# Performance work log

Measured on AMD Instinct MI355X. Metric: run time of the kernel, lower is better.

The kernel has to match this reference:

```python
import jax, jax.numpy as jnp
import numpy as np

N = 50000
E = 800000
D = 128
L = 2


def setup_inputs() -> dict:
    key = jax.random.key(0)
    ks = jax.random.split(key, 8)
    x = jax.random.normal(ks[0], (N, D), dtype=jnp.float32)
    edge_index = jax.random.randint(ks[1], (2, E), 0, N, dtype=jnp.int64)
    s = 1.0 / np.sqrt(D)
    Wl = jax.random.uniform(ks[2], (L, D, D), jnp.float32, -s, s)  # neighbor transform (with bias)
    bl = jax.random.uniform(ks[3], (L, D), jnp.float32, -s, s)
    Wr = jax.random.uniform(ks[4], (L, D, D), jnp.float32, -s, s)  # root/self transform (no bias)
    W = jax.random.uniform(ks[5], (D, D), jnp.float32, -s, s)      # final Linear
    b = jax.random.uniform(ks[6], (D,), jnp.float32, -s, s)
    return {"x": x, "edge_index": edge_index, "Wl": Wl, "bl": bl, "Wr": Wr, "W": W, "b": b}


def reference(x, edge_index, Wl, bl, Wr, W, b):
    src, dst = edge_index[0], edge_index[1]
    n = x.shape[0]
    for l in range(Wl.shape[0]):
        # gather neighbor (source) features, scatter-max into destination nodes
        agg = jax.ops.segment_max(x[src], dst, num_segments=n)  # [N, D]
        agg = jnp.where(jnp.isneginf(agg), 0.0, agg)  # PyG: isolated nodes -> 0
        # SAGEConv: lin_l(agg) + lin_r(x)
        x = agg @ Wl[l].T + bl[l] + x @ Wr[l].T
        x = jax.nn.relu(x)
    return x @ W.T + b
```

## Files before the change

### kernel.cpp

```cpp
#include <hip/hip_runtime.h>
#include <math.h>

#define NN 50000
#define NE 800000
#define DD 128
#define NBUCK 196
#define PTILE 4096
#define PBLOCKS 196
#define CONVB 6250
#define LHS 136

typedef unsigned short u16;
typedef short s8v __attribute__((ext_vector_type(8)));
typedef float f16v __attribute__((ext_vector_type(16)));

__device__ __forceinline__ u16 f2bf(float f) {
    unsigned u = __float_as_uint(f);
    return (u16)((u + 0x7FFFu + ((u >> 16) & 1u)) >> 16);
}
__device__ __forceinline__ float bflo(unsigned u) { return __uint_as_float(u << 16); }
__device__ __forceinline__ float bfhi(unsigned u) { return __uint_as_float(u & 0xFFFF0000u); }

__device__ __forceinline__ void pack_one(const float* __restrict__ Wl,
                                         const float* __restrict__ Wr,
                                         bool two, int o, u16* __restrict__ out) {
    int j = o & 7;
    int l = (o >> 3) & 63;
    int cn = o >> 9;
    int n = cn & 3;
    int c = cn >> 2;
    int colj = n * 32 + (l & 31);
    int k = c * 16 + (l >> 5) * 8 + j;
    float v;
    if (two) v = (k < DD) ? Wl[colj * DD + k] : Wr[colj * DD + (k - DD)];
    else     v = Wl[colj * DD + k];
    out[o] = f2bf(v);
}

__global__ __launch_bounds__(256) void prep_kernel(
        const int* __restrict__ ei, int* __restrict__ bcnt,
        const float4* __restrict__ x4, ushort4* __restrict__ hbx,
        const float* __restrict__ Wl, const float* __restrict__ Wr,
        const float* __restrict__ W,
        u16* __restrict__ Bpk0, u16* __restrict__ Bpk1, u16* __restrict__ Bpkf) {
    int bid = blockIdx.x;
    int tid = threadIdx.x;
    if (bid < PBLOCKS) {
        __shared__ int h[NBUCK];
        for (int i = tid; i < NBUCK; i += 256) h[i] = 0;
        __syncthreads();
        int e0 = bid * PTILE;
#pragma unroll
        for (int i = 0; i < 16; i++) {
            int e = e0 + i * 256 + tid;
            if (e < NE) atomicAdd(&h[ei[NE + e] >> 8], 1);
        }
        __syncthreads();
        for (int i = tid; i < NBUCK; i += 256)
            if (h[i]) atomicAdd(&bcnt[i], h[i]);
    } else if (bid < PBLOCKS + CONVB) {
        int i = (bid - PBLOCKS) * 256 + tid;
        float4 v = x4[i];
        ushort4 o;
        o.x = f2bf(v.x); o.y = f2bf(v.y); o.z = f2bf(v.z); o.w = f2bf(v.w);
        hbx[i] = o;
    } else if (bid < PBLOCKS + CONVB + 128) {
        pack_one(Wl, Wr, true, (bid - PBLOCKS - CONVB) * 256 + tid, Bpk0);
    } else if (bid < PBLOCKS + CONVB + 256) {
        pack_one(Wl + DD * DD, Wr + DD * DD, true, (bid - PBLOCKS - CONVB - 128) * 256 + tid, Bpk1);
    } else {
        pack_one(W, W, false, (bid - PBLOCKS - CONVB - 256) * 256 + tid, Bpkf);
    }
}

__global__ __launch_bounds__(256) void bucket_scan(const int* __restrict__ bcnt,
                                                   int* __restrict__ bbase,
                                                   int* __restrict__ bcur,
                                                   int* __restrict__ rowptr) {
    __shared__ int s[256];
    int t = threadIdx.x;
    int v = (t < NBUCK) ? bcnt[t] : 0;
    s[t] = v;
    __syncthreads();
    for (int o = 1; o < 256; o <<= 1) {
        int u = (t >= o) ? s[t - o] : 0;
        __syncthreads();
        s[t] += u;
        __syncthreads();
    }
    int ex = s[t] - v;
    if (t < NBUCK) { bbase[t] = ex; bcur[t] = ex; }
    if (t == 0) rowptr[NN] = NE;
}

__global__ __launch_bounds__(256) void bucket_partition(const int* __restrict__ ei,
                                                        int* __restrict__ bcur,
                                                        unsigned* __restrict__ packed) {
    __shared__ int h[NBUCK];
    __shared__ int base[NBUCK];
    int t = threadIdx.x;
    for (int i = t; i < NBUCK; i += 256) h[i] = 0;
    __syncthreads();
    int e0 = blockIdx.x * PTILE;
    int dsts[16], srcs[16];
#pragma unroll
    for (int i = 0; i < 16; i++) {
        int e = e0 + i * 256 + t;
        if (e < NE) {
            dsts[i] = ei[NE + e];
            srcs[i] = ei[e];
            atomicAdd(&h[dsts[i] >> 8], 1);
        } else dsts[i] = -1;
    }
    __syncthreads();
    for (int i = t; i < NBUCK; i += 256) {
        int c = h[i];
        base[i] = c ? atomicAdd(&bcur[i], c) : 0;
    }
    __syncthreads();
    for (int i = t; i < NBUCK; i += 256) h[i] = 0;
    __syncthreads();
#pragma unroll
    for (int i = 0; i < 16; i++) {
        if (dsts[i] >= 0) {
            int bk = dsts[i] >> 8;
            int r = atomicAdd(&h[bk], 1);
            packed[base[bk] + r] = (unsigned)srcs[i] | ((unsigned)(dsts[i] & 255) << 16);
        }
    }
}

__global__ __launch_bounds__(256) void bucket_csr(const unsigned* __restrict__ packed,
                                                  const int* __restrict__ bcnt,
                                                  const int* __restrict__ bbase,
                                                  int* __restrict__ rowptr,
                                                  int* __restrict__ col,
                                                  int* __restrict__ perm) {
    __shared__ int deg[256];
    __shared__ int off[256];
    __shared__ int dh[64];
    __shared__ int ds64[64];
    int bk = blockIdx.x;
    int cnt = bcnt[bk], base = bbase[bk];
    int t = threadIdx.x;
    deg[t] = 0;
    if (t < 64) dh[t] = 0;
    __syncthreads();
    for (int i = t; i < cnt; i += 256) atomicAdd(&deg[packed[base + i] >> 16], 1);
    __syncthreads();
    int v = deg[t];
    off[t] = v;
    __syncthreads();
    for (int o = 1; o < 256; o <<= 1) {
        int u = (t >= o) ? off[t - o] : 0;
        __syncthreads();
        off[t] += u;
        __syncthreads();
    }
    int ex = off[t] - v;
    int node = (bk << 8) + t;
    bool valid = node < NN;
    if (valid) rowptr[node] = base + ex;
    deg[t] = ex;
    int dcl = valid ? min(v, 63) : 0;
    int rank = atomicAdd(&dh[dcl], 1);
    __syncthreads();
    for (int i = t; i < cnt; i += 256) {
        unsigned p = packed[base + i];
        int dl = p >> 16;
        int r = atomicAdd(&deg[dl], 1);
        col[base + r] = (int)(p & 0xFFFFu);
    }
    if (t < 64) ds64[t] = dh[t];
    __syncthreads();
    for (int o = 1; o < 64; o <<= 1) {
        int u = (t >= o && t < 64) ? ds64[t - o] : 0;
        __syncthreads();
        if (t < 64) ds64[t] += u;
        __syncthreads();
    }
    int pos = ds64[dcl] - dh[dcl] + rank;
    perm[(bk << 8) + pos] = node;
}

__device__ __forceinline__ void vmax8(float* m, uint4 v) {
    m[0] = fmaxf(m[0], bflo(v.x)); m[1] = fmaxf(m[1], bfhi(v.x));
    m[2] = fmaxf(m[2], bflo(v.y)); m[3] = fmaxf(m[3], bfhi(v.y));
    m[4] = fmaxf(m[4], bflo(v.z)); m[5] = fmaxf(m[5], bfhi(v.z));
    m[6] = fmaxf(m[6], bflo(v.w)); m[7] = fmaxf(m[7], bfhi(v.w));
}

__global__ __launch_bounds__(256) void agg_kernel_bf(const uint4* __restrict__ xb4,
                                                     const int* __restrict__ row_ptr,
                                                     const int* __restrict__ col,
                                                     const int* __restrict__ perm,
                                                     uint4* __restrict__ aggb4) {
    int slot = blockIdx.x * 16 + (threadIdx.x >> 4);
    int node = perm[slot];
    if (node >= NN) return;
    int j = threadIdx.x & 15;
    int s0 = row_ptr[node], s1 = row_ptr[node + 1];
    if (s0 == s1) {
        aggb4[(size_t)node * 16 + j] = make_uint4(0, 0, 0, 0);
        return;
    }
    float m0[8], m1[8], m2[8], m3[8];
#pragma unroll
    for (int q = 0; q < 8; q++) { m0[q] = m1[q] = m2[q] = m3[q] = -INFINITY; }
    int i = s0;
    for (; i + 8 <= s1; i += 8) {
        int c0 = col[i],     c1 = col[i + 1], c2 = col[i + 2], c3 = col[i + 3];
        int c4 = col[i + 4], c5 = col[i + 5], c6 = col[i + 6], c7 = col[i + 7];
        uint4 v0 = xb4[(size_t)c0 * 16 + j];
        uint4 v1 = xb4[(size_t)c1 * 16 + j];
        uint4 v2 = xb4[(size_t)c2 * 16 + j];
        uint4 v3 = xb4[(size_t)c3 * 16 + j];
        uint4 v4 = xb4[(size_t)c4 * 16 + j];
        uint4 v5 = xb4[(size_t)c5 * 16 + j];
        uint4 v6 = xb4[(size_t)c6 * 16 + j];
        uint4 v7 = xb4[(size_t)c7 * 16 + j];
        vmax8(m0, v0); vmax8(m1, v1); vmax8(m2, v2); vmax8(m3, v3);
        vmax8(m0, v4); vmax8(m1, v5); vmax8(m2, v6); vmax8(m3, v7);
    }
    for (; i + 4 <= s1; i += 4) {
        int c0 = col[i], c1 = col[i + 1], c2 = col[i + 2], c3 = col[i + 3];
        uint4 v0 = xb4[(size_t)c0 * 16 + j];
        uint4 v1 = xb4[(size_t)c1 * 16 + j];
        uint4 v2 = xb4[(size_t)c2 * 16 + j];
        uint4 v3 = xb4[(size_t)c3 * 16 + j];
        vmax8(m0, v0); vmax8(m1, v1); vmax8(m2, v2); vmax8(m3, v3);
    }
    for (; i < s1; i++) {
        uint4 v = xb4[(size_t)col[i] * 16 + j];
        vmax8(m0, v);
    }
#pragma unroll
    for (int q = 0; q < 8; q++) m0[q] = fmaxf(fmaxf(m0[q], m1[q]), fmaxf(m2[q], m3[q]));
    uint4 o;
    o.x = (__float_as_uint(m0[0]) >> 16) | (__float_as_uint(m0[1]) & 0xFFFF0000u);
    o.y = (__float_as_uint(m0[2]) >> 16) | (__float_as_uint(m0[3]) & 0xFFFF0000u);
    o.z = (__float_as_uint(m0[4]) >> 16) | (__float_as_uint(m0[5]) & 0xFFFF0000u);
    o.w = (__float_as_uint(m0[6]) >> 16) | (__float_as_uint(m0[7]) & 0xFFFF0000u);
    aggb4[(size_t)node * 16 + j] = o;
}

__global__ __launch_bounds__(256) void mfma_gemm0(const u16* __restrict__ srcA,
                                                  const u16* __restrict__ srcB,
                                                  const u16* __restrict__ Bpk,
                                                  const float* __restrict__ bias,
                                                  u16* __restrict__ outb) {
    int tid = threadIdx.x;
    int wt = tid >> 6;
    int lane = tid & 63;
    int row0 = blockIdx.x * 128 + wt * 32;
    int rload = row0 + (lane & 31);
    if (rload > NN - 1) rload = NN - 1;
    int koff = (lane >> 5) * 8;
    const s8v* Bv = (const s8v*)Bpk;

    f16v acc[4];
#pragma unroll
    for (int n = 0; n < 4; n++) acc[n] = (f16v)(0.0f);

#pragma unroll
    for (int c = 0; c < 16; c++) {
        const u16* s = (c >= 8) ? srcB : srcA;
        int kk = (c >= 8) ? (c - 8) * 16 : c * 16;
        s8v a = *(const s8v*)(s + (size_t)rload * DD + kk + koff);
#pragma unroll
        for (int n = 0; n < 4; n++) {
            s8v b = Bv[(c * 4 + n) * 64 + lane];
            acc[n] = __builtin_amdgcn_mfma_f32_32x32x16_bf16(a, b, acc[n], 0, 0, 0);
        }
    }

    int rowadd = 4 * (lane >> 5);
#pragma unroll
    for (int n = 0; n < 4; n++) {
        int colj = n * 32 + (lane & 31);
        float bj = bias[colj];
#pragma unroll
        for (int r = 0; r < 16; r++) {
            int row = row0 + (r & 3) + 8 * (r >> 2) + rowadd;
            if (row < NN) outb[(size_t)row * DD + colj] = f2bf(fmaxf(acc[n][r] + bj, 0.0f));
        }
    }
}

__global__ __launch_bounds__(256) void mfma_gemm1_final(const u16* __restrict__ srcA,
                                                        const u16* __restrict__ srcB,
                                                        const u16* __restrict__ Bpk1,
                                                        const float* __restrict__ bias1,
                                                        const u16* __restrict__ Bpkf,
                                                        const float* __restrict__ bias2,
                                                        float* __restrict__ out) {
    __shared__ u16 lh[128 * LHS];
    int tid = threadIdx.x;
    int wt = tid >> 6;
    int lane = tid & 63;
    int row0 = blockIdx.x * 128 + wt * 32;
    int rload = row0 + (lane & 31);
    if (rload > NN - 1) rload = NN - 1;
    int koff = (lane >> 5) * 8;
    const s8v* Bv1 = (const s8v*)Bpk1;
    const s8v* Bvf = (const s8v*)Bpkf;

    f16v acc[4];
#pragma unroll
    for (int n = 0; n < 4; n++) acc[n] = (f16v)(0.0f);

#pragma unroll
    for (int c = 0; c < 16; c++) {
        const u16* s = (c >= 8) ? srcB : srcA;
        int kk = (c >= 8) ? (c - 8) * 16 : c * 16;
        s8v a = *(const s8v*)(s + (size_t)rload * DD + kk + koff);
#pragma unroll
        for (int n = 0; n < 4; n++) {
            s8v b = Bv1[(c * 4 + n) * 64 + lane];
            acc[n] = __builtin_amdgcn_mfma_f32_32x32x16_bf16(a, b, acc[n], 0, 0, 0);
        }
    }

    int rowadd = 4 * (lane >> 5);
#pragma unroll
    for (int n = 0; n < 4; n++) {
        int colj = n * 32 + (lane & 31);
        float bj = bias1[colj];
#pragma unroll
        for (int r = 0; r < 16; r++) {
            int rl = (r & 3) + 8 * (r >> 2) + rowadd;
            lh[(wt * 32 + rl) * LHS + colj] = f2bf(fmaxf(acc[n][r] + bj, 0.0f));
        }
    }
    __syncthreads();

    f16v acc2[4];
#pragma unroll
    for (int n = 0; n < 4; n++) acc2[n] = (f16v)(0.0f);
    int m = lane & 31;
#pragma unroll
    for (int c = 0; c < 8; c++) {
        s8v a = *(const s8v*)&lh[(wt * 32 + m) * LHS + c * 16 + koff];
#pragma unroll
        for (int n = 0; n < 4; n++) {
            s8v b = Bvf[(c * 4 + n) * 64 + lane];
            acc2[n] = __builtin_amdgcn_mfma_f32_32x32x16_bf16(a, b, acc2[n], 0, 0, 0);
        }
    }

#pragma unroll
    for (int n = 0; n < 4; n++) {
        int colj = n * 32 + (lane & 31);
        float bj = bias2[colj];
#pragma unroll
        for (int r = 0; r < 16; r++) {
            int row = row0 + (r & 3) + 8 * (r >> 2) + rowadd;
            if (row < NN) out[(size_t)row * DD + colj] = acc2[n][r] + bj;
        }
    }
}

extern "C" void kernel_launch(void* const* d_in, const int* in_sizes, int n_in,
                              void* d_out, int out_size, void* d_ws, size_t ws_size,
                              hipStream_t stream) {
    const float* x  = (const float*)d_in[0];
    const int*   ei = (const int*)d_in[1];
    const float* Wl = (const float*)d_in[2];
    const float* bl = (const float*)d_in[3];
    const float* Wr = (const float*)d_in[4];
    const float* W  = (const float*)d_in[5];
    const float* b  = (const float*)d_in[6];
    float* out = (float*)d_out;

    u16* aggb = (u16*)d_ws;
    u16* hbx  = aggb + (size_t)NN * DD;
    u16* h1   = hbx + (size_t)NN * DD;
    u16* Bpk0 = h1 + (size_t)NN * DD;
    u16* Bpk1 = Bpk0 + 32768;
    u16* Bpkf = Bpk1 + 32768;
    unsigned* packed = (unsigned*)(Bpkf + 16384);
    int* col    = (int*)(packed + NE);
    int* rowptr = col + NE;
    int* perm   = rowptr + NN + 1;
    int* bcnt   = perm + NBUCK * 256;
    int* bbase  = bcnt + NBUCK;
    int* bcur   = bbase + NBUCK;

    dim3 blk(256);
    int gemmBlocks = (NN + 127) / 128;
    int aggBlocks  = NBUCK * 256 / 16;
    int prepBlocks = PBLOCKS + CONVB + 320;

    hipMemsetAsync(bcnt, 0, NBUCK * sizeof(int), stream);

    prep_kernel<<<prepBlocks, blk, 0, stream>>>(
        ei, bcnt, (const float4*)x, (ushort4*)hbx, Wl, Wr, W, Bpk0, Bpk1, Bpkf);

    bucket_scan<<<1, blk, 0, stream>>>(bcnt, bbase, bcur, rowptr);
    bucket_partition<<<PBLOCKS, blk, 0, stream>>>(ei, bcur, packed);
    bucket_csr<<<NBUCK, blk, 0, stream>>>(packed, bcnt, bbase, rowptr, col, perm);

    agg_kernel_bf<<<aggBlocks, blk, 0, stream>>>((const uint4*)hbx, rowptr, col, perm, (uint4*)aggb);
    mfma_gemm0<<<gemmBlocks, blk, 0, stream>>>(aggb, hbx, Bpk0, bl, h1);

    agg_kernel_bf<<<aggBlocks, blk, 0, stream>>>((const uint4*)h1, rowptr, col, perm, (uint4*)aggb);
    mfma_gemm1_final<<<gemmBlocks, blk, 0, stream>>>(aggb, h1, Bpk1, bl + DD, Bpkf, b, out);
}
```

Baseline: 253.1 us.

## Slice aggregation by feature quarter and drop degree-sorted node permutation

```diff
diff --git a/kernel.cpp b/kernel.cpp
--- a/kernel.cpp
+++ b/kernel.cpp
@@ -8,11 +8,14 @@
 #define PTILE 4096
 #define PBLOCKS 196
 #define CONVB 6250
+#define ASLICE 4
+#define ABLK 782
 #define LHS 136
 
 typedef unsigned short u16;
 typedef short s8v __attribute__((ext_vector_type(8)));
 typedef float f16v __attribute__((ext_vector_type(16)));
+typedef unsigned u32x4 __attribute__((ext_vector_type(4)));
 
 __device__ __forceinline__ u16 f2bf(float f) {
     unsigned u = __float_as_uint(f);
@@ -38,39 +41,44 @@
 }
 
 __global__ __launch_bounds__(256) void prep_kernel(
-        const int* __restrict__ ei, int* __restrict__ bcnt,
         const float4* __restrict__ x4, ushort4* __restrict__ hbx,
         const float* __restrict__ Wl, const float* __restrict__ Wr,
         const float* __restrict__ W,
-        u16* __restrict__ Bpk0, u16* __restrict__ Bpk1, u16* __restrict__ Bpkf) {
+        u16* __restrict__ Bpk0, u16* __restrict__ Bpk1, u16* __restrict__ Bpkf,
+        int* __restrict__ bcnt) {
     int bid = blockIdx.x;
     int tid = threadIdx.x;
-    if (bid < PBLOCKS) {
-        __shared__ int h[NBUCK];
-        for (int i = tid; i < NBUCK; i += 256) h[i] = 0;
-        __syncthreads();
-        int e0 = bid * PTILE;
-#pragma unroll
-        for (int i = 0; i < 16; i++) {
-            int e = e0 + i * 256 + tid;
-            if (e < NE) atomicAdd(&h[ei[NE + e] >> 8], 1);
-        }
-        __syncthreads();
-        for (int i = tid; i < NBUCK; i += 256)
-            if (h[i]) atomicAdd(&bcnt[i], h[i]);
-    } else if (bid < PBLOCKS + CONVB) {
-        int i = (bid - PBLOCKS) * 256 + tid;
+    if (bid < CONVB) {
+        int i = bid * 256 + tid;
         float4 v = x4[i];
         ushort4 o;
         o.x = f2bf(v.x); o.y = f2bf(v.y); o.z = f2bf(v.z); o.w = f2bf(v.w);
         hbx[i] = o;
-    } else if (bid < PBLOCKS + CONVB + 128) {
-        pack_one(Wl, Wr, true, (bid - PBLOCKS - CONVB) * 256 + tid, Bpk0);
-    } else if (bid < PBLOCKS + CONVB + 256) {
-        pack_one(Wl + DD * DD, Wr + DD * DD, true, (bid - PBLOCKS - CONVB - 128) * 256 + tid, Bpk1);
+    } else if (bid < CONVB + 128) {
+        pack_one(Wl, Wr, true, (bid - CONVB) * 256 + tid, Bpk0);
+    } else if (bid < CONVB + 256) {
+        pack_one(Wl + DD * DD, Wr + DD * DD, true, (bid - CONVB - 128) * 256 + tid, Bpk1);
+    } else if (bid < CONVB + 320) {
+        pack_one(W, W, false, (bid - CONVB - 256) * 256 + tid, Bpkf);
     } else {
-        pack_one(W, W, false, (bid - PBLOCKS - CONVB - 256) * 256 + tid, Bpkf);
-    }
+        if (tid < NBUCK) bcnt[tid] = 0;
+    }
+}
+
+__global__ __launch_bounds__(256) void bucket_hist(const int* __restrict__ ei,
+                                                   int* __restrict__ bcnt) {
+    __shared__ int h[NBUCK];
+    for (int i = threadIdx.x; i < NBUCK; i += 256) h[i] = 0;
+    __syncthreads();
+    int e0 = blockIdx.x * PTILE;
+#pragma unroll
+    for (int i = 0; i < 16; i++) {
+        int e = e0 + i * 256 + threadIdx.x;
+        if (e < NE) atomicAdd(&h[ei[NE + e] >> 8], 1);
+    }
+    __syncthreads();
+    for (int i = threadIdx.x; i < NBUCK; i += 256)
+        if (h[i]) atomicAdd(&bcnt[i], h[i]);
 }
 
 __global__ __launch_bounds__(256) void bucket_scan(const int* __restrict__ bcnt,
@@ -134,17 +142,13 @@
                                                   const int* __restrict__ bcnt,
                                                   const int* __restrict__ bbase,
                                                   int* __restrict__ rowptr,
-                                                  int* __restrict__ col,
-                                                  int* __restrict__ perm) {
+                                                  int* __restrict__ col) {
     __shared__ int deg[256];
     __shared__ int off[256];
-    __shared__ int dh[64];
-    __shared__ int ds64[64];
     int bk = blockIdx.x;
     int cnt = bcnt[bk], base = bbase[bk];
     int t = threadIdx.x;
     deg[t] = 0;
-    if (t < 64) dh[t] = 0;
     __syncthreads();
     for (int i = t; i < cnt; i += 256) atomicAdd(&deg[packed[base + i] >> 16], 1);
     __syncthreads();
@@ -159,11 +163,8 @@
     }
     int ex = off[t] - v;
     int node = (bk << 8) + t;
-    bool valid = node < NN;
-    if (valid) rowptr[node] = base + ex;
+    if (node < NN) rowptr[node] = base + ex;
     deg[t] = ex;
-    int dcl = valid ? min(v, 63) : 0;
-    int rank = atomicAdd(&dh[dcl], 1);
     __syncthreads();
     for (int i = t; i < cnt; i += 256) {
         unsigned p = packed[base + i];
@@ -171,37 +172,30 @@
         int r = atomicAdd(&deg[dl], 1);
         col[base + r] = (int)(p & 0xFFFFu);
     }
-    if (t < 64) ds64[t] = dh[t];
-    __syncthreads();
-    for (int o = 1; o < 64; o <<= 1) {
-        int u = (t >= o && t < 64) ? ds64[t - o] : 0;
-        __syncthreads();
-        if (t < 64) ds64[t] += u;
-        __syncthreads();
-    }
-    int pos = ds64[dcl] - dh[dcl] + rank;
-    perm[(bk << 8) + pos] = node;
-}
-
-__device__ __forceinline__ void vmax8(float* m, uint4 v) {
+}
+
+__device__ __forceinline__ void vmax8(float* m, u32x4 v) {
     m[0] = fmaxf(m[0], bflo(v.x)); m[1] = fmaxf(m[1], bfhi(v.x));
     m[2] = fmaxf(m[2], bflo(v.y)); m[3] = fmaxf(m[3], bfhi(v.y));
     m[4] = fmaxf(m[4], bflo(v.z)); m[5] = fmaxf(m[5], bfhi(v.z));
     m[6] = fmaxf(m[6], bflo(v.w)); m[7] = fmaxf(m[7], bfhi(v.w));
 }
 
-__global__ __launch_bounds__(256) void agg_kernel_bf(const uint4* __restrict__ xb4,
+__global__ __launch_bounds__(256) void agg_kernel_bf(const u32x4* __restrict__ xb4,
                                                      const int* __restrict__ row_ptr,
                                                      const int* __restrict__ col,
-                                                     const int* __restrict__ perm,
-                                                     uint4* __restrict__ aggb4) {
-    int slot = blockIdx.x * 16 + (threadIdx.x >> 4);
-    int node = perm[slot];
+                                                     u32x4* __restrict__ aggb4) {
+    int bid = blockIdx.x;
+    int slice = bid / ABLK;
+    int blk = bid - slice * ABLK;
+    int node = blk * 64 + (threadIdx.x >> 2);
     if (node >= NN) return;
-    int j = threadIdx.x & 15;
+    int j = (threadIdx.x & 3) + slice * 4;
     int s0 = row_ptr[node], s1 = row_ptr[node + 1];
+    u32x4* outp = aggb4 + (size_t)node * 16 + j;
     if (s0 == s1) {
-        aggb4[(size_t)node * 16 + j] = make_uint4(0, 0, 0, 0);
+        u32x4 z = (u32x4)(0u);
+        __builtin_nontemporal_store(z, outp);
         return;
     }
     float m0[8], m1[8], m2[8], m3[8];
@@ -209,39 +203,49 @@
     for (int q = 0; q < 8; q++) { m0[q] = m1[q] = m2[q] = m3[q] = -INFINITY; }
     int i = s0;
     for (; i + 8 <= s1; i += 8) {
-        int c0 = col[i],     c1 = col[i + 1], c2 = col[i + 2], c3 = col[i + 3];
-        int c4 = col[i + 4], c5 = col[i + 5], c6 = col[i + 6], c7 = col[i + 7];
-        uint4 v0 = xb4[(size_t)c0 * 16 + j];
-        uint4 v1 = xb4[(size_t)c1 * 16 + j];
-        uint4 v2 = xb4[(size_t)c2 * 16 + j];
-        uint4 v3 = xb4[(size_t)c3 * 16 + j];
-        uint4 v4 = xb4[(size_t)c4 * 16 + j];
-        uint4 v5 = xb4[(size_t)c5 * 16 + j];
-        uint4 v6 = xb4[(size_t)c6 * 16 + j];
-        uint4 v7 = xb4[(size_t)c7 * 16 + j];
+        int c0 = __builtin_nontemporal_load(&col[i]);
+        int c1 = __builtin_nontemporal_load(&col[i + 1]);
+        int c2 = __builtin_nontemporal_load(&col[i + 2]);
+        int c3 = __builtin_nontemporal_load(&col[i + 3]);
+        int c4 = __builtin_nontemporal_load(&col[i + 4]);
+        int c5 = __builtin_nontemporal_load(&col[i + 5]);
+        int c6 = __builtin_nontemporal_load(&col[i + 6]);
+        int c7 = __builtin_nontemporal_load(&col[i + 7]);
+        u32x4 v0 = xb4[(size_t)c0 * 16 + j];
+        u32x4 v1 = xb4[(size_t)c1 * 16 + j];
+        u32x4 v2 = xb4[(size_t)c2 * 16 + j];
+        u32x4 v3 = xb4[(size_t)c3 * 16 + j];
+        u32x4 v4 = xb4[(size_t)c4 * 16 + j];
+        u32x4 v5 = xb4[(size_t)c5 * 16 + j];
+        u32x4 v6 = xb4[(size_t)c6 * 16 + j];
+        u32x4 v7 = xb4[(size_t)c7 * 16 + j];
         vmax8(m0, v0); vmax8(m1, v1); vmax8(m2, v2); vmax8(m3, v3);
         vmax8(m0, v4); vmax8(m1, v5); vmax8(m2, v6); vmax8(m3, v7);
     }
     for (; i + 4 <= s1; i += 4) {
-        int c0 = col[i], c1 = col[i + 1], c2 = col[i + 2], c3 = col[i + 3];
-        uint4 v0 = xb4[(size_t)c0 * 16 + j];
-        uint4 v1 = xb4[(size_t)c1 * 16 + j];
-        uint4 v2 = xb4[(size_t)c2 * 16 + j];
-        uint4 v3 = xb4[(size_t)c3 * 16 + j];
+        int c0 = __builtin_nontemporal_load(&col[i]);
+        int c1 = __builtin_nontemporal_load(&col[i + 1]);
+        int c2 = __builtin_nontemporal_load(&col[i + 2]);
+        int c3 = __builtin_nontemporal_load(&col[i + 3]);
+        u32x4 v0 = xb4[(size_t)c0 * 16 + j];
+        u32x4 v1 = xb4[(size_t)c1 * 16 + j];
+        u32x4 v2 = xb4[(size_t)c2 * 16 + j];
+        u32x4 v3 = xb4[(size_t)c3 * 16 + j];
         vmax8(m0, v0); vmax8(m1, v1); vmax8(m2, v2); vmax8(m3, v3);
     }
     for (; i < s1; i++) {
-        uint4 v = xb4[(size_t)col[i] * 16 + j];
+        int c0 = __builtin_nontemporal_load(&col[i]);
+        u32x4 v = xb4[(size_t)c0 * 16 + j];
         vmax8(m0, v);
     }
 #pragma unroll
     for (int q = 0; q < 8; q++) m0[q] = fmaxf(fmaxf(m0[q], m1[q]), fmaxf(m2[q], m3[q]));
-    uint4 o;
+    u32x4 o;
     o.x = (__float_as_uint(m0[0]) >> 16) | (__float_as_uint(m0[1]) & 0xFFFF0000u);
     o.y = (__float_as_uint(m0[2]) >> 16) | (__float_as_uint(m0[3]) & 0xFFFF0000u);
     o.z = (__float_as_uint(m0[4]) >> 16) | (__float_as_uint(m0[5]) & 0xFFFF0000u);
     o.w = (__float_as_uint(m0[6]) >> 16) | (__float_as_uint(m0[7]) & 0xFFFF0000u);
-    aggb4[(size_t)node * 16 + j] = o;
+    __builtin_nontemporal_store(o, outp);
 }
 
 __global__ __launch_bounds__(256) void mfma_gemm0(const u16* __restrict__ srcA,
@@ -381,28 +385,26 @@
     unsigned* packed = (unsigned*)(Bpkf + 16384);
     int* col    = (int*)(packed + NE);
     int* rowptr = col + NE;
-    int* perm   = rowptr + NN + 1;
-    int* bcnt   = perm + NBUCK * 256;
+    int* bcnt   = rowptr + NN + 1;
     int* bbase  = bcnt + NBUCK;
     int* bcur   = bbase + NBUCK;
 
     dim3 blk(256);
     int gemmBlocks = (NN + 127) / 128;
-    int aggBlocks  = NBUCK * 256 / 16;
-    int prepBlocks = PBLOCKS + CONVB + 320;
-
-    hipMemsetAsync(bcnt, 0, NBUCK * sizeof(int), stream);
+    int aggBlocks  = ASLICE * ABLK;
+    int prepBlocks = CONVB + 320 + 1;
 
     prep_kernel<<<prepBlocks, blk, 0, stream>>>(
-        ei, bcnt, (const float4*)x, (ushort4*)hbx, Wl, Wr, W, Bpk0, Bpk1, Bpkf);
-
+        (const float4*)x, (ushort4*)hbx, Wl, Wr, W, Bpk0, Bpk1, Bpkf, bcnt);
+
+    bucket_hist<<<PBLOCKS, blk, 0, stream>>>(ei, bcnt);
     bucket_scan<<<1, blk, 0, stream>>>(bcnt, bbase, bcur, rowptr);
     bucket_partition<<<PBLOCKS, blk, 0, stream>>>(ei, bcur, packed);
-    bucket_csr<<<NBUCK, blk, 0, stream>>>(packed, bcnt, bbase, rowptr, col, perm);
-
-    agg_kernel_bf<<<aggBlocks, blk, 0, stream>>>((const uint4*)hbx, rowptr, col, perm, (uint4*)aggb);
+    bucket_csr<<<NBUCK, blk, 0, stream>>>(packed, bcnt, bbase, rowptr, col);
+
+    agg_kernel_bf<<<aggBlocks, blk, 0, stream>>>((const u32x4*)hbx, rowptr, col, (u32x4*)aggb);
     mfma_gemm0<<<gemmBlocks, blk, 0, stream>>>(aggb, hbx, Bpk0, bl, h1);
 
-    agg_kernel_bf<<<aggBlocks, blk, 0, stream>>>((const uint4*)h1, rowptr, col, perm, (uint4*)aggb);
+    agg_kernel_bf<<<aggBlocks, blk, 0, stream>>>((const u32x4*)h1, rowptr, col, (u32x4*)aggb);
     mfma_gemm1_final<<<gemmBlocks, blk, 0, stream>>>(aggb, h1, Bpk1, bl + DD, Bpkf, b, out);
 }
```

After: 278.0 us. 1.1x slower.
